# Kernel optimization log

Measured on AMD Instinct MI355X. Metric: run time of the kernel, lower is better.

## Reference

```python
import jax, jax.numpy as jnp
import numpy as np

B, S, H_DIM = 2, 2048, 1024
N_HEADS, HEAD_DIM = 16, 64
EPS = 1e-6


def phi(x):
    return jax.nn.elu(x) + 1.0


def setup_inputs() -> dict:
    key = jax.random.key(0)
    ks = jax.random.split(key, 11)
    std = 0.02
    proj = N_HEADS * HEAD_DIM
    return {
        "query": jax.random.normal(ks[0], (B, S, H_DIM), dtype=jnp.float32),
        "key": jax.random.normal(ks[1], (B, S, H_DIM), dtype=jnp.float32),
        "value": jax.random.normal(ks[2], (B, S, H_DIM), dtype=jnp.float32),
        "Wq": jax.random.normal(ks[3], (proj, H_DIM), dtype=jnp.float32) * std,
        "bq": jnp.zeros((proj,), dtype=jnp.float32),
        "Wk": jax.random.normal(ks[4], (proj, H_DIM), dtype=jnp.float32) * std,
        "bk": jnp.zeros((proj,), dtype=jnp.float32),
        "Wv": jax.random.normal(ks[5], (proj, H_DIM), dtype=jnp.float32) * std,
        "bv": jnp.zeros((proj,), dtype=jnp.float32),
        "Wo": jax.random.normal(ks[6], (H_DIM, proj), dtype=jnp.float32) * std,
        "bo": jnp.zeros((H_DIM,), dtype=jnp.float32),
    }


def reference(query, key, value, Wq, bq, Wk, bk, Wv, bv, Wo, bo):
    b, s, _ = query.shape
    # QKV projections (torch nn.Linear: y = x @ W.T + b)
    q = query @ Wq.T + bq
    k = key @ Wk.T + bk
    v = value @ Wv.T + bv
    # (b, s, h*d) -> (b, h, s, d)
    def split_heads(t):
        return t.reshape(b, s, N_HEADS, HEAD_DIM).transpose(0, 2, 1, 3)
    q, k, v = split_heads(q), split_heads(k), split_heads(v)

    q_phi = phi(q)  # (b,h,s,d)
    k_phi = phi(k)

    # cumulative outer products: (b,h,s,d_k,d_v)
    kv = k_phi[..., :, None] * v[..., None, :]
    kv_cumsum = jnp.cumsum(kv, axis=2)
    k_phi_cumsum = jnp.cumsum(k_phi, axis=2)

    out_num = jnp.einsum('bhsd,bhsdj->bhsj', q_phi, kv_cumsum)
    out_den = jnp.einsum('bhsd,bhsd->bhs', q_phi, k_phi_cumsum)
    out = out_num / (out_den[..., None] + EPS)

    out = out.transpose(0, 2, 1, 3).reshape(b, s, N_HEADS * HEAD_DIM)
    return out @ Wo.T + bo
```

## Files before the change

kernel.cpp:

```cpp
#include <hip/hip_runtime.h>
#include <hip/hip_bf16.h>
#include <stdint.h>

typedef __bf16 bf16x8 __attribute__((ext_vector_type(8)));
typedef float  f32x4  __attribute__((ext_vector_type(4)));
typedef __hip_bfloat16 hbf16;

#define AS1 __attribute__((address_space(1)))
#define AS3 __attribute__((address_space(3)))

__device__ __forceinline__ void gload_lds16(const void* g, void* l) {
  __builtin_amdgcn_global_load_lds((const AS1 void*)g, (AS3 void*)l, 16, 0, 0);
}

__device__ __forceinline__ f32x4 mfma_bf16(bf16x8 a, bf16x8 b, f32x4 c) {
  return __builtin_amdgcn_mfma_f32_16x16x32_bf16(a, b, c, 0, 0, 0);
}


__global__ __launch_bounds__(256) void convert_all(
    const float* __restrict__ q, const float* __restrict__ k, const float* __restrict__ v,
    const float* __restrict__ wq, const float* __restrict__ wk,
    const float* __restrict__ wv, const float* __restrict__ wo,
    hbf16* __restrict__ dst)
{
  const int i8 = (blockIdx.x * 256 + threadIdx.x) * 8;
  const float* src;
  int off;
  if      (i8 < (4  << 20)) { src = q;  off = i8; }
  else if (i8 < (8  << 20)) { src = k;  off = i8 - (4  << 20); }
  else if (i8 < (12 << 20)) { src = v;  off = i8 - (8  << 20); }
  else if (i8 < (13 << 20)) { src = wq; off = i8 - (12 << 20); }
  else if (i8 < (14 << 20)) { src = wk; off = i8 - (13 << 20); }
  else if (i8 < (15 << 20)) { src = wv; off = i8 - (14 << 20); }
  else                      { src = wo; off = i8 - (15 << 20); }
  const float4 a = *(const float4*)(src + off);
  const float4 b = *(const float4*)(src + off + 4);
  hbf16 h[8];
  h[0] = __float2bfloat16(a.x); h[1] = __float2bfloat16(a.y);
  h[2] = __float2bfloat16(a.z); h[3] = __float2bfloat16(a.w);
  h[4] = __float2bfloat16(b.x); h[5] = __float2bfloat16(b.y);
  h[6] = __float2bfloat16(b.z); h[7] = __float2bfloat16(b.w);
  *(uint4*)(dst + i8) = *(uint4*)h;
}

__device__ __forceinline__ void gemm_core_128(
    const hbf16* __restrict__ A, const hbf16* __restrict__ Bw,
    int by, int bx, hbf16* sA, hbf16* sB, f32x4 (&acc)[4][4])
{
  const int tid  = threadIdx.x;
  const int lane = tid & 63;
  const int wid  = tid >> 6;
  const int wm = wid >> 1, wn = wid & 1;
  const int l15 = lane & 15, l4 = lane >> 4;
  const int K = 1024;

  auto STAGE = [&](int kt) {
    const int k0 = kt * 64;
    #pragma unroll
    for (int j = 0; j < 4; ++j) {
      const int o   = (j * 256 + tid) * 16;
      const int row = o >> 7;
      const int csw = (o & 127) ^ ((row & 7) << 4);
      gload_lds16((const char*)A  + ((size_t)(by * 128 + row) * K + k0) * 2 + csw,
                  (char*)sA + o);
      gload_lds16((const char*)Bw + ((size_t)(bx * 128 + row) * K + k0) * 2 + csw,
                  (char*)sB + o);
    }
  };

  STAGE(0);
  for (int kt = 0; kt < 16; ++kt) {
    __syncthreads();
    bf16x8 af[2][4], bfr[2][4];
    #pragma unroll
    for (int kk = 0; kk < 2; ++kk) {
      #pragma unroll
      for (int m = 0; m < 4; ++m) {
        const int row = wm * 64 + m * 16 + l15;
        const int col = (kk * 64 + l4 * 16) ^ ((row & 7) << 4);
        af[kk][m] = *(const bf16x8*)((const char*)sA + row * 128 + col);
      }
      #pragma unroll
      for (int n = 0; n < 4; ++n) {
        const int row = wn * 64 + n * 16 + l15;
        const int col = (kk * 64 + l4 * 16) ^ ((row & 7) << 4);
        bfr[kk][n] = *(const bf16x8*)((const char*)sB + row * 128 + col);
      }
    }
    __syncthreads();
    if (kt < 15) STAGE(kt + 1);
    __builtin_amdgcn_sched_barrier(0);
    #pragma unroll
    for (int kk = 0; kk < 2; ++kk) {
      #pragma unroll
      for (int m = 0; m < 4; ++m) {
        #pragma unroll
        for (int n = 0; n < 4; ++n) {
          acc[m][n] = mfma_bf16(af[kk][m], bfr[kk][n], acc[m][n]);
        }
      }
    }
  }
}

__device__ __forceinline__ void xcd_remap(int& bx, int& by) {
  const int X = blockIdx.x, Y = blockIdx.y;
  by = X * 4 + (Y & 3);
  bx = Y >> 2;
}

__global__ __launch_bounds__(256, 3) void qkv_gemm(
    const hbf16* __restrict__ qin, const hbf16* __restrict__ kin, const hbf16* __restrict__ vin,
    const hbf16* __restrict__ wq, const hbf16* __restrict__ wk, const hbf16* __restrict__ wv,
    const float* __restrict__ bq, const float* __restrict__ bk, const float* __restrict__ bv,
    hbf16* __restrict__ q_phi, hbf16* __restrict__ k_phi,
    hbf16* __restrict__ kphiT, hbf16* __restrict__ vT)
{
  const int z = blockIdx.z;
  const hbf16* A    = (z == 0) ? qin : (z == 1) ? kin : vin;
  const hbf16* W    = (z == 0) ? wq  : (z == 1) ? wk  : wv;
  const float* bias = (z == 0) ? bq  : (z == 1) ? bk  : bv;

  int bx, by;
  xcd_remap(bx, by);

  __shared__ hbf16 sA[128 * 64];
  __shared__ hbf16 sB[128 * 64];
  f32x4 acc[4][4] = {};
  gemm_core_128(A, W, by, bx, sA, sB, acc);

  const int tid = threadIdx.x, lane = tid & 63, wid = tid >> 6;
  const int wm = wid >> 1, wn = wid & 1, l15 = lane & 15, l4 = lane >> 4;

  #pragma unroll
  for (int n = 0; n < 4; ++n) {
    const int gn = bx * 128 + wn * 64 + n * 16 + l15;
    const float bs = bias[gn];
    const int h = gn >> 6, dd = gn & 63;
    #pragma unroll
    for (int m = 0; m < 4; ++m) {
      #pragma unroll
      for (int j = 0; j < 4; ++j) {
        const int gm = by * 128 + wm * 64 + m * 16 + l4 * 4 + j;
        const int b = gm >> 11, s = gm & 2047;
        float val = acc[m][n][j] + bs;
        if (z < 2) val = (val > 0.f) ? (val + 1.f) : __expf(val);
        const hbf16 hv = __float2bfloat16(val);
        const int bh = b * 16 + h;
        if (z == 0) {
          q_phi[((size_t)bh * 2048 + s) * 64 + dd] = hv;
        } else if (z == 1) {
          k_phi[((size_t)bh * 2048 + s) * 64 + dd] = hv;
          kphiT[((size_t)bh * 32 + (s >> 6)) * 4096 + dd * 64 + (s & 63)] = hv;
        } else {
          vT[((size_t)bh * 32 + (s >> 6)) * 4096 + dd * 64 + (s & 63)] = hv;
        }
      }
    }
  }
}

__global__ __launch_bounds__(256) void chunk_sums(
    const hbf16* __restrict__ kphiT, const hbf16* __restrict__ vT,
    float* __restrict__ sums)
{
  const int c = blockIdx.x, bh = blockIdx.y;
  const int tid = threadIdx.x, lane = tid & 63, w = tid >> 6;
  const int l15 = lane & 15, l4 = lane >> 4;
  const size_t tbase = ((size_t)bh * 32 + c) * 4096;

  f32x4 acc[5] = {};
  #pragma unroll
  for (int kk = 0; kk < 2; ++kk) {
    const bf16x8 bfr = *(const bf16x8*)&kphiT[tbase + (w * 16 + l15) * 64 + l4 * 8 + kk * 32];
    #pragma unroll
    for (int mj = 0; mj < 5; ++mj) {
      bf16x8 af;
      if (mj < 4) {
        af = *(const bf16x8*)&vT[tbase + (mj * 16 + l15) * 64 + l4 * 8 + kk * 32];
      } else {
        const __bf16 e = (l15 == 0) ? (__bf16)1.0f : (__bf16)0.0f;
        #pragma unroll
        for (int i = 0; i < 8; ++i) af[i] = e;
      }
      acc[mj] = mfma_bf16(af, bfr, acc[mj]);
    }
  }
  float* outp = sums + ((size_t)bh * 32 + c) * 5120;
  #pragma unroll
  for (int mj = 0; mj < 5; ++mj) {
    #pragma unroll
    for (int j = 0; j < 4; ++j) {
      outp[(mj * 16 + l4 * 4 + j) * 64 + w * 16 + l15] = acc[mj][j];
    }
  }
}

__global__ __launch_bounds__(256) void chunk_scan(
    const float* __restrict__ sums, hbf16* __restrict__ pre)
{
  const int elem = blockIdx.x * 256 + threadIdx.x;
  const int bh = blockIdx.y;
  const size_t base = (size_t)bh * 32 * 5120 + elem;
  float v[32];
  #pragma unroll
  for (int c = 0; c < 32; ++c) v[c] = sums[base + (size_t)c * 5120];
  float run = 0.f;
  #pragma unroll
  for (int c = 0; c < 32; ++c) {
    pre[base + (size_t)c * 5120] = __float2bfloat16(run);
    run += v[c];
  }
}

__global__ __launch_bounds__(256) void attn_chunk(
    const hbf16* __restrict__ q_phi, const hbf16* __restrict__ k_phi,
    const hbf16* __restrict__ vT, const hbf16* __restrict__ pre,
    hbf16* __restrict__ attn)
{
  const int c = blockIdx.x, bh = blockIdx.y;
  const int tid = threadIdx.x, lane = tid & 63, w = tid >> 6;
  const int l15 = lane & 15, l4 = lane >> 4;
  __shared__ hbf16 sS[4 * 16 * 64];

  const size_t qbase = ((size_t)bh * 2048 + c * 64) * 64;
  const size_t tbase = ((size_t)bh * 32 + c) * 4096;
  const size_t pbase = ((size_t)bh * 32 + c) * 5120;

  bf16x8 aq[2];
  #pragma unroll
  for (int kk = 0; kk < 2; ++kk)
    aq[kk] = *(const bf16x8*)&q_phi[qbase + (w * 16 + l15) * 64 + l4 * 8 + kk * 32];

  f32x4 accS[4] = {};
  #pragma unroll
  for (int kk = 0; kk < 2; ++kk) {
    #pragma unroll
    for (int ni = 0; ni < 4; ++ni) {
      const bf16x8 bk = *(const bf16x8*)&k_phi[qbase + (ni * 16 + l15) * 64 + l4 * 8 + kk * 32];
      accS[ni] = mfma_bf16(aq[kk], bk, accS[ni]);
    }
  }
  #pragma unroll
  for (int ni = 0; ni < 4; ++ni) {
    #pragma unroll
    for (int j = 0; j < 4; ++j) {
      const int r  = l4 * 4 + j;
      const int cc = ni * 16 + l15;
      const float v = (cc <= w * 16 + r) ? accS[ni][j] : 0.f;
      sS[w * 1024 + r * 64 + (cc ^ ((r & 7) << 3))] = __float2bfloat16(v);
    }
  }

  f32x4 accN[5] = {};
  #pragma unroll
  for (int kk = 0; kk < 2; ++kk) {
    const bf16x8 aS = *(const bf16x8*)&sS[w * 1024 + l15 * 64 +
                                          ((l4 * 8 + kk * 32) ^ ((l15 & 7) << 3))];
    #pragma unroll
    for (int ni = 0; ni < 5; ++ni) {
      bf16x8 bv;
      if (ni < 4) {
        bv = *(const bf16x8*)&vT[tbase + (ni * 16 + l15) * 64 + l4 * 8 + kk * 32];
      } else {
        const __bf16 e = (l15 == 0) ? (__bf16)1.0f : (__bf16)0.0f;
        #pragma unroll
        for (int i = 0; i < 8; ++i) bv[i] = e;
      }
      accN[ni] = mfma_bf16(aS, bv, accN[ni]);
    }
  }
  #pragma unroll
  for (int kk = 0; kk < 2; ++kk) {
    #pragma unroll
    for (int ni = 0; ni < 5; ++ni) {
      const bf16x8 bp = *(const bf16x8*)&pre[pbase + (ni * 16 + l15) * 64 + l4 * 8 + kk * 32];
      accN[ni] = mfma_bf16(aq[kk], bp, accN[ni]);
    }
  }
  const int b = bh >> 4, h = bh & 15;
  #pragma unroll
  for (int j = 0; j < 4; ++j) {
    const float den = __shfl(accN[4][j], lane & 48);
    const float inv = 1.f / (den + 1e-6f);
    const int sg = c * 64 + w * 16 + l4 * 4 + j;
    #pragma unroll
    for (int ni = 0; ni < 4; ++ni) {
      attn[((size_t)b * 2048 + sg) * 1024 + h * 64 + ni * 16 + l15] =
          __float2bfloat16(accN[ni][j] * inv);
    }
  }
}

__global__ __launch_bounds__(256, 3) void out_gemm(
    const hbf16* __restrict__ attn, const hbf16* __restrict__ wo,
    const float* __restrict__ bo, float* __restrict__ out)
{
  int bx, by;
  xcd_remap(bx, by);

  __shared__ hbf16 sA[128 * 64];
  __shared__ hbf16 sB[128 * 64];
  f32x4 acc[4][4] = {};
  gemm_core_128(attn, wo, by, bx, sA, sB, acc);

  const int tid = threadIdx.x, lane = tid & 63, wid = tid >> 6;
  const int wm = wid >> 1, wn = wid & 1, l15 = lane & 15, l4 = lane >> 4;
  #pragma unroll
  for (int n = 0; n < 4; ++n) {
    const int gn = bx * 128 + wn * 64 + n * 16 + l15;
    const float bs = bo[gn];
    #pragma unroll
    for (int m = 0; m < 4; ++m) {
      #pragma unroll
      for (int j = 0; j < 4; ++j) {
        const int gm = by * 128 + wm * 64 + m * 16 + l4 * 4 + j;
        out[(size_t)gm * 1024 + gn] = acc[m][n][j] + bs;
      }
    }
  }
}

extern "C" void kernel_launch(void* const* d_in, const int* in_sizes, int n_in,
                              void* d_out, int out_size, void* d_ws, size_t ws_size,
                              hipStream_t stream) {
  const float* q  = (const float*)d_in[0];
  const float* k  = (const float*)d_in[1];
  const float* v  = (const float*)d_in[2];
  const float* Wq = (const float*)d_in[3];
  const float* bq = (const float*)d_in[4];
  const float* Wk = (const float*)d_in[5];
  const float* bk = (const float*)d_in[6];
  const float* Wv = (const float*)d_in[7];
  const float* bv = (const float*)d_in[8];
  const float* Wo = (const float*)d_in[9];
  const float* bo = (const float*)d_in[10];

  char* ws = (char*)d_ws;
  const size_t MB = (size_t)1 << 20;
  hbf16* qin  = (hbf16*)(ws + 0 * MB);
  hbf16* kin  = (hbf16*)(ws + 8 * MB);
  hbf16* vin  = (hbf16*)(ws + 16 * MB);
  hbf16* wqb  = (hbf16*)(ws + 24 * MB);
  hbf16* wkb  = (hbf16*)(ws + 26 * MB);
  hbf16* wvb  = (hbf16*)(ws + 28 * MB);
  hbf16* wob  = (hbf16*)(ws + 30 * MB);
  hbf16* qphi = (hbf16*)(ws + 32 * MB);
  hbf16* kphi = (hbf16*)(ws + 40 * MB);
  hbf16* kphT = (hbf16*)(ws + 48 * MB);
  hbf16* vTb  = (hbf16*)(ws + 56 * MB);
  hbf16* attn = (hbf16*)(ws + 64 * MB);
  float* sums = (float*)(ws + 72 * MB);
  hbf16* pre  = (hbf16*)(ws + 92 * MB);

  convert_all<<<8192, 256, 0, stream>>>(q, k, v, Wq, Wk, Wv, Wo, qin);
  qkv_gemm<<<dim3(8, 32, 3), 256, 0, stream>>>(qin, kin, vin, wqb, wkb, wvb,
                                               bq, bk, bv, qphi, kphi, kphT, vTb);
  chunk_sums<<<dim3(32, 32), 256, 0, stream>>>(kphT, vTb, sums);
  chunk_scan<<<dim3(20, 32), 256, 0, stream>>>(sums, pre);
  attn_chunk<<<dim3(32, 32), 256, 0, stream>>>(qphi, kphi, vTb, pre, attn);
  out_gemm<<<dim3(8, 32), 256, 0, stream>>>(attn, wob, bo, (float*)d_out);
}
```

Baseline: 201.4 us.

## Use 64x128 double-buffered GEMM tiles with async prefetch in QKV and output GEMMs

```diff
diff --git a/kernel.cpp b/kernel.cpp
--- a/kernel.cpp
+++ b/kernel.cpp
@@ -44,70 +44,89 @@
   *(uint4*)(dst + i8) = *(uint4*)h;
 }
 
-__device__ __forceinline__ void gemm_core_128(
+template<int NKT>
+__device__ __forceinline__ void gemm_core_64x128(
     const hbf16* __restrict__ A, const hbf16* __restrict__ Bw,
-    int by, int bx, hbf16* sA, hbf16* sB, f32x4 (&acc)[4][4])
+    int by, int bx, hbf16* sA, hbf16* sB, f32x4 (&acc)[4][2])
 {
   const int tid  = threadIdx.x;
   const int lane = tid & 63;
   const int wid  = tid >> 6;
-  const int wm = wid >> 1, wn = wid & 1;
-  const int l15 = lane & 15, l4 = lane >> 4;
-  const int K = 1024;
-
-  auto STAGE = [&](int kt) {
+  const int l15 = lane & 15, l4 = lane >> 4;
+  const int K = NKT * 64;
+
+  auto STAGE = [&](int kt, int buf) {
     const int k0 = kt * 64;
+    #pragma unroll
+    for (int j = 0; j < 2; ++j) {
+      const int o   = (j * 256 + tid) * 16;
+      const int row = o >> 7;
+      const int csw = (o & 127) ^ ((row & 7) << 4);
+      gload_lds16((const char*)A + ((size_t)(by * 64 + row) * K + k0) * 2 + csw,
+                  (char*)(sA + buf * 64 * 64) + o);
+    }
     #pragma unroll
     for (int j = 0; j < 4; ++j) {
       const int o   = (j * 256 + tid) * 16;
       const int row = o >> 7;
       const int csw = (o & 127) ^ ((row & 7) << 4);
-      gload_lds16((const char*)A  + ((size_t)(by * 128 + row) * K + k0) * 2 + csw,
-                  (char*)sA + o);
       gload_lds16((const char*)Bw + ((size_t)(bx * 128 + row) * K + k0) * 2 + csw,
-                  (char*)sB + o);
+                  (char*)(sB + buf * 128 * 64) + o);
     }
   };
 
-  STAGE(0);
-  for (int kt = 0; kt < 16; ++kt) {
-    __syncthreads();
-    bf16x8 af[2][4], bfr[2][4];
+  STAGE(0, 0);
+  STAGE(1, 1);
+  #pragma unroll
+  for (int kt = 0; kt < NKT; ++kt) {
+    const int buf = kt & 1;
+    if (kt < NKT - 1) asm volatile("s_waitcnt vmcnt(6)" ::: "memory");
+    else              asm volatile("s_waitcnt vmcnt(0)" ::: "memory");
+    __builtin_amdgcn_s_barrier();
+    __builtin_amdgcn_sched_barrier(0);
+
+    bf16x8 af[2][4], bfr[2][2];
+    const hbf16* bA = sA + buf * 64 * 64;
+    const hbf16* bB = sB + buf * 128 * 64;
     #pragma unroll
     for (int kk = 0; kk < 2; ++kk) {
       #pragma unroll
       for (int m = 0; m < 4; ++m) {
-        const int row = wm * 64 + m * 16 + l15;
+        const int row = m * 16 + l15;
         const int col = (kk * 64 + l4 * 16) ^ ((row & 7) << 4);
-        af[kk][m] = *(const bf16x8*)((const char*)sA + row * 128 + col);
-      }
-      #pragma unroll
-      for (int n = 0; n < 4; ++n) {
-        const int row = wn * 64 + n * 16 + l15;
+        af[kk][m] = *(const bf16x8*)((const char*)bA + row * 128 + col);
+      }
+      #pragma unroll
+      for (int n = 0; n < 2; ++n) {
+        const int row = wid * 32 + n * 16 + l15;
         const int col = (kk * 64 + l4 * 16) ^ ((row & 7) << 4);
-        bfr[kk][n] = *(const bf16x8*)((const char*)sB + row * 128 + col);
-      }
-    }
-    __syncthreads();
-    if (kt < 15) STAGE(kt + 1);
+        bfr[kk][n] = *(const bf16x8*)((const char*)bB + row * 128 + col);
+      }
+    }
+    asm volatile("s_waitcnt lgkmcnt(0)" ::: "memory");
     __builtin_amdgcn_sched_barrier(0);
-    #pragma unroll
-    for (int kk = 0; kk < 2; ++kk) {
-      #pragma unroll
-      for (int m = 0; m < 4; ++m) {
+    if (kt + 2 < NKT) {
+      __builtin_amdgcn_s_barrier();
+      __builtin_amdgcn_sched_barrier(0);
+      STAGE(kt + 2, buf);
+      __builtin_amdgcn_sched_barrier(0);
+    }
+    __builtin_amdgcn_s_setprio(1);
+    #pragma unroll
+    for (int kk = 0; kk < 2; ++kk)
+      #pragma unroll
+      for (int m = 0; m < 4; ++m)
         #pragma unroll
-        for (int n = 0; n < 4; ++n) {
+        for (int n = 0; n < 2; ++n)
           acc[m][n] = mfma_bf16(af[kk][m], bfr[kk][n], acc[m][n]);
-        }
-      }
-    }
+    __builtin_amdgcn_s_setprio(0);
   }
 }
 
 __device__ __forceinline__ void xcd_remap(int& bx, int& by) {
   const int X = blockIdx.x, Y = blockIdx.y;
-  by = X * 4 + (Y & 3);
-  bx = Y >> 2;
+  by = X * 8 + (Y & 7);
+  bx = Y >> 3;
 }
 
 __global__ __launch_bounds__(256, 3) void qkv_gemm(
@@ -125,24 +144,24 @@
   int bx, by;
   xcd_remap(bx, by);
 
-  __shared__ hbf16 sA[128 * 64];
-  __shared__ hbf16 sB[128 * 64];
-  f32x4 acc[4][4] = {};
-  gemm_core_128(A, W, by, bx, sA, sB, acc);
+  __shared__ hbf16 sA[2 * 64 * 64];
+  __shared__ hbf16 sB[2 * 128 * 64];
+  f32x4 acc[4][2] = {};
+  gemm_core_64x128<16>(A, W, by, bx, sA, sB, acc);
 
   const int tid = threadIdx.x, lane = tid & 63, wid = tid >> 6;
-  const int wm = wid >> 1, wn = wid & 1, l15 = lane & 15, l4 = lane >> 4;
-
-  #pragma unroll
-  for (int n = 0; n < 4; ++n) {
-    const int gn = bx * 128 + wn * 64 + n * 16 + l15;
+  const int l15 = lane & 15, l4 = lane >> 4;
+
+  #pragma unroll
+  for (int n = 0; n < 2; ++n) {
+    const int gn = bx * 128 + wid * 32 + n * 16 + l15;
     const float bs = bias[gn];
     const int h = gn >> 6, dd = gn & 63;
     #pragma unroll
     for (int m = 0; m < 4; ++m) {
       #pragma unroll
       for (int j = 0; j < 4; ++j) {
-        const int gm = by * 128 + wm * 64 + m * 16 + l4 * 4 + j;
+        const int gm = by * 64 + m * 16 + l4 * 4 + j;
         const int b = gm >> 11, s = gm & 2047;
         float val = acc[m][n][j] + bs;
         if (z < 2) val = (val > 0.f) ? (val + 1.f) : __expf(val);
@@ -300,22 +319,22 @@
   int bx, by;
   xcd_remap(bx, by);
 
-  __shared__ hbf16 sA[128 * 64];
-  __shared__ hbf16 sB[128 * 64];
-  f32x4 acc[4][4] = {};
-  gemm_core_128(attn, wo, by, bx, sA, sB, acc);
+  __shared__ hbf16 sA[2 * 64 * 64];
+  __shared__ hbf16 sB[2 * 128 * 64];
+  f32x4 acc[4][2] = {};
+  gemm_core_64x128<16>(attn, wo, by, bx, sA, sB, acc);
 
   const int tid = threadIdx.x, lane = tid & 63, wid = tid >> 6;
-  const int wm = wid >> 1, wn = wid & 1, l15 = lane & 15, l4 = lane >> 4;
-  #pragma unroll
-  for (int n = 0; n < 4; ++n) {
-    const int gn = bx * 128 + wn * 64 + n * 16 + l15;
+  const int l15 = lane & 15, l4 = lane >> 4;
+  #pragma unroll
+  for (int n = 0; n < 2; ++n) {
+    const int gn = bx * 128 + wid * 32 + n * 16 + l15;
     const float bs = bo[gn];
     #pragma unroll
     for (int m = 0; m < 4; ++m) {
       #pragma unroll
       for (int j = 0; j < 4; ++j) {
-        const int gm = by * 128 + wm * 64 + m * 16 + l4 * 4 + j;
+        const int gm = by * 64 + m * 16 + l4 * 4 + j;
         out[(size_t)gm * 1024 + gn] = acc[m][n][j] + bs;
       }
     }
@@ -355,10 +374,10 @@
   hbf16* pre  = (hbf16*)(ws + 92 * MB);
 
   convert_all<<<8192, 256, 0, stream>>>(q, k, v, Wq, Wk, Wv, Wo, qin);
-  qkv_gemm<<<dim3(8, 32, 3), 256, 0, stream>>>(qin, kin, vin, wqb, wkb, wvb,
+  qkv_gemm<<<dim3(8, 64, 3), 256, 0, stream>>>(qin, kin, vin, wqb, wkb, wvb,
                                                bq, bk, bv, qphi, kphi, kphT, vTb);
   chunk_sums<<<dim3(32, 32), 256, 0, stream>>>(kphT, vTb, sums);
   chunk_scan<<<dim3(20, 32), 256, 0, stream>>>(sums, pre);
   attn_chunk<<<dim3(32, 32), 256, 0, stream>>>(qphi, kphi, vTb, pre, attn);
-  out_gemm<<<dim3(8, 32), 256, 0, stream>>>(attn, wob, bo, (float*)d_out);
-}
+  out_gemm<<<dim3(8, 64), 256, 0, stream>>>(attn, wob, bo, (float*)d_out);
+}
```

New measurement: 206.0 us. 1.02x slower.

## Replace QKV projection with 256x256-tile double-buffered 8-wave pipelined GEMM

Applied to the files above, without the earlier changes.

```diff
diff --git a/kernel.cpp b/kernel.cpp
--- a/kernel.cpp
+++ b/kernel.cpp
@@ -44,6 +44,162 @@
   *(uint4*)(dst + i8) = *(uint4*)h;
 }
 
+#define NKT_Q 16
+
+__global__ __launch_bounds__(512, 2) void qkv_gemm256(
+    const hbf16* __restrict__ qin, const hbf16* __restrict__ kin, const hbf16* __restrict__ vin,
+    const hbf16* __restrict__ wq, const hbf16* __restrict__ wk, const hbf16* __restrict__ wv,
+    const float* __restrict__ bq, const float* __restrict__ bk, const float* __restrict__ bv,
+    hbf16* __restrict__ q_phi, hbf16* __restrict__ k_phi,
+    hbf16* __restrict__ kphiT, hbf16* __restrict__ vT)
+{
+  const int p  = blockIdx.x + (blockIdx.y << 2) + (blockIdx.z << 6);
+  const int L  = (p & 7) * 24 + (p >> 3);
+  const int z  = L >> 6;
+  const int rem = L & 63;
+  const int by = rem >> 2;
+  const int bx = rem & 3;
+
+  const hbf16* A    = (z == 0) ? qin : (z == 1) ? kin : vin;
+  const hbf16* W    = (z == 0) ? wq  : (z == 1) ? wk  : wv;
+  const float* bias = (z == 0) ? bq  : (z == 1) ? bk  : bv;
+
+  __shared__ hbf16 sA[2 * 256 * 64];
+  __shared__ hbf16 sB[2 * 256 * 64];
+
+  const int tid  = threadIdx.x;
+  const int lane = tid & 63;
+  const int wid  = tid >> 6;
+  const int wm   = wid >> 2;
+  const int wn   = wid & 3;
+  const int l15  = lane & 15, l4 = lane >> 4;
+  const int K = 1024;
+
+  auto STAGEQ = [&](const hbf16* G, hbf16* S, int gRowBase, int t, int q) {
+    const int o   = tid * 16;
+    const int row = o >> 7;
+    const int csw = (o & 127) ^ ((row & 7) << 4);
+    gload_lds16((const char*)G + ((size_t)(gRowBase + q * 64 + row) * K + t * 64) * 2 + csw,
+                (char*)(S + (t & 1) * (256 * 64) + q * (64 * 64)) + o);
+  };
+
+  f32x4 acc[4][2][4] = {};
+
+  #pragma unroll
+  for (int q = 0; q < 4; ++q) STAGEQ(A, sA, by * 256, 0, q);
+  #pragma unroll
+  for (int q = 0; q < 4; ++q) STAGEQ(W, sB, bx * 256, 0, q);
+  #pragma unroll
+  for (int q = 0; q < 4; ++q) STAGEQ(W, sB, bx * 256, 1, q);
+  STAGEQ(A, sA, by * 256, 1, 0);
+  STAGEQ(A, sA, by * 256, 1, 1);
+  asm volatile("s_waitcnt vmcnt(6)" ::: "memory");
+  __builtin_amdgcn_s_barrier();
+
+  for (int kt = 0; kt < NKT_Q; kt += 2) {
+    #pragma unroll
+    for (int half = 0; half < 2; ++half) {
+      const int t = kt + half;
+      const hbf16* bufA = sA + (t & 1) * (256 * 64);
+      const hbf16* bufB = sB + (t & 1) * (256 * 64);
+      bf16x8 bf[4][2];
+      #pragma unroll
+      for (int pph = 0; pph < 4; ++pph) {
+        if (pph == 0) {
+          #pragma unroll
+          for (int n = 0; n < 4; ++n)
+            #pragma unroll
+            for (int kk = 0; kk < 2; ++kk) {
+              const int row = wn * 64 + n * 16 + l15;
+              const int col = (kk * 64 + l4 * 16) ^ ((row & 7) << 4);
+              bf[n][kk] = *(const bf16x8*)((const char*)bufB + row * 128 + col);
+            }
+        }
+        bf16x8 af[2][2];
+        #pragma unroll
+        for (int i = 0; i < 2; ++i)
+          #pragma unroll
+          for (int kk = 0; kk < 2; ++kk) {
+            const int row = pph * 64 + wm * 32 + i * 16 + l15;
+            const int col = (kk * 64 + l4 * 16) ^ ((row & 7) << 4);
+            af[i][kk] = *(const bf16x8*)((const char*)bufA + row * 128 + col);
+          }
+        if (half == 0) {
+          if (pph == 0) {
+            STAGEQ(A, sA, by * 256, kt + 1, 2);
+            STAGEQ(A, sA, by * 256, kt + 1, 3);
+          } else if (kt + 2 < NKT_Q) {
+            if (pph == 1) { STAGEQ(W, sB, bx * 256, kt + 2, 0); STAGEQ(W, sB, bx * 256, kt + 2, 1); }
+            if (pph == 2) { STAGEQ(W, sB, bx * 256, kt + 2, 2); STAGEQ(W, sB, bx * 256, kt + 2, 3); }
+            if (pph == 3) { STAGEQ(A, sA, by * 256, kt + 2, 0); STAGEQ(A, sA, by * 256, kt + 2, 1); }
+          }
+        } else {
+          if (pph == 0) {
+            if (kt + 2 < NKT_Q) {
+              STAGEQ(A, sA, by * 256, kt + 2, 2);
+              STAGEQ(A, sA, by * 256, kt + 2, 3);
+            }
+          } else if (kt + 3 < NKT_Q) {
+            if (pph == 1) { STAGEQ(W, sB, bx * 256, kt + 3, 0); STAGEQ(W, sB, bx * 256, kt + 3, 1); }
+            if (pph == 2) { STAGEQ(W, sB, bx * 256, kt + 3, 2); STAGEQ(W, sB, bx * 256, kt + 3, 3); }
+            if (pph == 3) { STAGEQ(A, sA, by * 256, kt + 3, 0); STAGEQ(A, sA, by * 256, kt + 3, 1); }
+          }
+        }
+        __builtin_amdgcn_s_barrier();
+        asm volatile("s_waitcnt lgkmcnt(0)" ::: "memory");
+        __builtin_amdgcn_s_setprio(1);
+        #pragma unroll
+        for (int i = 0; i < 2; ++i)
+          #pragma unroll
+          for (int n = 0; n < 4; ++n)
+            #pragma unroll
+            for (int kk = 0; kk < 2; ++kk)
+              acc[pph][i][n] = mfma_bf16(af[i][kk], bf[n][kk], acc[pph][i][n]);
+        __builtin_amdgcn_s_setprio(0);
+        if (pph == 3) {
+          if (half == 0) {
+            if (kt + 2 < NKT_Q) asm volatile("s_waitcnt vmcnt(6)" ::: "memory");
+            else                asm volatile("s_waitcnt vmcnt(0)" ::: "memory");
+          } else {
+            if (kt + 2 < NKT_Q) asm volatile("s_waitcnt vmcnt(6)" ::: "memory");
+          }
+        }
+        __builtin_amdgcn_s_barrier();
+      }
+    }
+  }
+
+  #pragma unroll
+  for (int n = 0; n < 4; ++n) {
+    const int gn = bx * 256 + wn * 64 + n * 16 + l15;
+    const float bs = bias[gn];
+    const int h = gn >> 6, dd = gn & 63;
+    #pragma unroll
+    for (int pph = 0; pph < 4; ++pph) {
+      #pragma unroll
+      for (int i = 0; i < 2; ++i) {
+        #pragma unroll
+        for (int j = 0; j < 4; ++j) {
+          const int gm = by * 256 + pph * 64 + wm * 32 + i * 16 + l4 * 4 + j;
+          const int b = gm >> 11, s = gm & 2047;
+          float val = acc[pph][i][n][j] + bs;
+          if (z < 2) val = (val > 0.f) ? (val + 1.f) : __expf(val);
+          const hbf16 hv = __float2bfloat16(val);
+          const int bh = b * 16 + h;
+          if (z == 0) {
+            q_phi[((size_t)bh * 2048 + s) * 64 + dd] = hv;
+          } else if (z == 1) {
+            k_phi[((size_t)bh * 2048 + s) * 64 + dd] = hv;
+            kphiT[((size_t)bh * 32 + (s >> 6)) * 4096 + dd * 64 + (s & 63)] = hv;
+          } else {
+            vT[((size_t)bh * 32 + (s >> 6)) * 4096 + dd * 64 + (s & 63)] = hv;
+          }
+        }
+      }
+    }
+  }
+}
+
 __device__ __forceinline__ void gemm_core_128(
     const hbf16* __restrict__ A, const hbf16* __restrict__ Bw,
     int by, int bx, hbf16* sA, hbf16* sB, f32x4 (&acc)[4][4])
@@ -92,15 +248,12 @@
     if (kt < 15) STAGE(kt + 1);
     __builtin_amdgcn_sched_barrier(0);
     #pragma unroll
-    for (int kk = 0; kk < 2; ++kk) {
-      #pragma unroll
-      for (int m = 0; m < 4; ++m) {
-        #pragma unroll
-        for (int n = 0; n < 4; ++n) {
+    for (int kk = 0; kk < 2; ++kk)
+      #pragma unroll
+      for (int m = 0; m < 4; ++m)
+        #pragma unroll
+        for (int n = 0; n < 4; ++n)
           acc[m][n] = mfma_bf16(af[kk][m], bfr[kk][n], acc[m][n]);
-        }
-      }
-    }
   }
 }
 
@@ -108,57 +261,6 @@
   const int X = blockIdx.x, Y = blockIdx.y;
   by = X * 4 + (Y & 3);
   bx = Y >> 2;
-}
-
-__global__ __launch_bounds__(256, 3) void qkv_gemm(
-    const hbf16* __restrict__ qin, const hbf16* __restrict__ kin, const hbf16* __restrict__ vin,
-    const hbf16* __restrict__ wq, const hbf16* __restrict__ wk, const hbf16* __restrict__ wv,
-    const float* __restrict__ bq, const float* __restrict__ bk, const float* __restrict__ bv,
-    hbf16* __restrict__ q_phi, hbf16* __restrict__ k_phi,
-    hbf16* __restrict__ kphiT, hbf16* __restrict__ vT)
-{
-  const int z = blockIdx.z;
-  const hbf16* A    = (z == 0) ? qin : (z == 1) ? kin : vin;
-  const hbf16* W    = (z == 0) ? wq  : (z == 1) ? wk  : wv;
-  const float* bias = (z == 0) ? bq  : (z == 1) ? bk  : bv;
-
-  int bx, by;
-  xcd_remap(bx, by);
-
-  __shared__ hbf16 sA[128 * 64];
-  __shared__ hbf16 sB[128 * 64];
-  f32x4 acc[4][4] = {};
-  gemm_core_128(A, W, by, bx, sA, sB, acc);
-
-  const int tid = threadIdx.x, lane = tid & 63, wid = tid >> 6;
-  const int wm = wid >> 1, wn = wid & 1, l15 = lane & 15, l4 = lane >> 4;
-
-  #pragma unroll
-  for (int n = 0; n < 4; ++n) {
-    const int gn = bx * 128 + wn * 64 + n * 16 + l15;
-    const float bs = bias[gn];
-    const int h = gn >> 6, dd = gn & 63;
-    #pragma unroll
-    for (int m = 0; m < 4; ++m) {
-      #pragma unroll
-      for (int j = 0; j < 4; ++j) {
-        const int gm = by * 128 + wm * 64 + m * 16 + l4 * 4 + j;
-        const int b = gm >> 11, s = gm & 2047;
-        float val = acc[m][n][j] + bs;
-        if (z < 2) val = (val > 0.f) ? (val + 1.f) : __expf(val);
-        const hbf16 hv = __float2bfloat16(val);
-        const int bh = b * 16 + h;
-        if (z == 0) {
-          q_phi[((size_t)bh * 2048 + s) * 64 + dd] = hv;
-        } else if (z == 1) {
-          k_phi[((size_t)bh * 2048 + s) * 64 + dd] = hv;
-          kphiT[((size_t)bh * 32 + (s >> 6)) * 4096 + dd * 64 + (s & 63)] = hv;
-        } else {
-          vT[((size_t)bh * 32 + (s >> 6)) * 4096 + dd * 64 + (s & 63)] = hv;
-        }
-      }
-    }
-  }
 }
 
 __global__ __launch_bounds__(256) void chunk_sums(
@@ -355,8 +457,8 @@
   hbf16* pre  = (hbf16*)(ws + 92 * MB);
 
   convert_all<<<8192, 256, 0, stream>>>(q, k, v, Wq, Wk, Wv, Wo, qin);
-  qkv_gemm<<<dim3(8, 32, 3), 256, 0, stream>>>(qin, kin, vin, wqb, wkb, wvb,
-                                               bq, bk, bv, qphi, kphi, kphT, vTb);
+  qkv_gemm256<<<dim3(4, 16, 3), 512, 0, stream>>>(qin, kin, vin, wqb, wkb, wvb,
+                                                  bq, bk, bv, qphi, kphi, kphT, vTb);
   chunk_sums<<<dim3(32, 32), 256, 0, stream>>>(kphT, vTb, sums);
   chunk_scan<<<dim3(20, 32), 256, 0, stream>>>(sums, pre);
   attn_chunk<<<dim3(32, 32), 256, 0, stream>>>(qphi, kphi, vTb, pre, attn);
```

Measured after the change: 226.4 us. 12.4% more time.

## Stage QKV and attention epilogues through LDS for coalesced 16-byte stores

Applied to the files above, without the earlier changes.

```diff
diff --git a/kernel.cpp b/kernel.cpp
--- a/kernel.cpp
+++ b/kernel.cpp
@@ -92,15 +92,12 @@
     if (kt < 15) STAGE(kt + 1);
     __builtin_amdgcn_sched_barrier(0);
     #pragma unroll
-    for (int kk = 0; kk < 2; ++kk) {
-      #pragma unroll
-      for (int m = 0; m < 4; ++m) {
+    for (int kk = 0; kk < 2; ++kk)
+      #pragma unroll
+      for (int m = 0; m < 4; ++m)
         #pragma unroll
-        for (int n = 0; n < 4; ++n) {
+        for (int n = 0; n < 4; ++n)
           acc[m][n] = mfma_bf16(af[kk][m], bfr[kk][n], acc[m][n]);
-        }
-      }
-    }
   }
 }
 
@@ -125,38 +122,77 @@
   int bx, by;
   xcd_remap(bx, by);
 
-  __shared__ hbf16 sA[128 * 64];
-  __shared__ hbf16 sB[128 * 64];
+  __shared__ hbf16 smem[2 * 128 * 64];
   f32x4 acc[4][4] = {};
-  gemm_core_128(A, W, by, bx, sA, sB, acc);
+  gemm_core_128(A, W, by, bx, smem, smem + 128 * 64, acc);
 
   const int tid = threadIdx.x, lane = tid & 63, wid = tid >> 6;
   const int wm = wid >> 1, wn = wid & 1, l15 = lane & 15, l4 = lane >> 4;
-
-  #pragma unroll
-  for (int n = 0; n < 4; ++n) {
-    const int gn = bx * 128 + wn * 64 + n * 16 + l15;
-    const float bs = bias[gn];
-    const int h = gn >> 6, dd = gn & 63;
-    #pragma unroll
-    for (int m = 0; m < 4; ++m) {
-      #pragma unroll
-      for (int j = 0; j < 4; ++j) {
-        const int gm = by * 128 + wm * 64 + m * 16 + l4 * 4 + j;
-        const int b = gm >> 11, s = gm & 2047;
-        float val = acc[m][n][j] + bs;
-        if (z < 2) val = (val > 0.f) ? (val + 1.f) : __expf(val);
-        const hbf16 hv = __float2bfloat16(val);
-        const int bh = b * 16 + h;
-        if (z == 0) {
-          q_phi[((size_t)bh * 2048 + s) * 64 + dd] = hv;
-        } else if (z == 1) {
-          k_phi[((size_t)bh * 2048 + s) * 64 + dd] = hv;
-          kphiT[((size_t)bh * 32 + (s >> 6)) * 4096 + dd * 64 + (s & 63)] = hv;
-        } else {
-          vT[((size_t)bh * 32 + (s >> 6)) * 4096 + dd * 64 + (s & 63)] = hv;
+  const int b = by >> 4;
+
+  float bs[4];
+  #pragma unroll
+  for (int n = 0; n < 4; ++n) bs[n] = bias[bx * 128 + wn * 64 + n * 16 + l15];
+
+  auto finish = [&](float v) -> float {
+    return (z < 2) ? ((v > 0.f) ? (v + 1.f) : __expf(v)) : v;
+  };
+
+  if (z < 2) {
+    #pragma unroll
+    for (int n = 0; n < 4; ++n) {
+      const int col = wn * 64 + n * 16 + l15;
+      #pragma unroll
+      for (int m = 0; m < 4; ++m) {
+        #pragma unroll
+        for (int j = 0; j < 4; ++j) {
+          const int row = wm * 64 + m * 16 + l4 * 4 + j;
+          smem[row * 128 + (col ^ ((row & 7) << 3))] =
+              __float2bfloat16(finish(acc[m][n][j] + bs[n]));
         }
       }
+    }
+    __syncthreads();
+    hbf16* dst = (z == 0) ? q_phi : k_phi;
+    #pragma unroll
+    for (int it = 0; it < 8; ++it) {
+      const int sgi = it * 256 + tid;
+      const int sl = sgi >> 4, seg = sgi & 15;
+      const uint4 vv = *(const uint4*)&smem[sl * 128 + ((seg * 8) ^ ((sl & 7) << 3))];
+      const int gnb = bx * 128 + seg * 8;
+      const int h = gnb >> 6, dd = gnb & 63;
+      const int s = (by * 128 + sl) & 2047;
+      *(uint4*)&dst[(((size_t)(b * 16 + h)) * 2048 + s) * 64 + dd] = vv;
+    }
+  }
+  if (z >= 1) {
+    if (z == 1) __syncthreads();
+    #pragma unroll
+    for (int n = 0; n < 4; ++n) {
+      const int gnl = wn * 64 + n * 16 + l15;
+      const int x = (gnl & 7) << 3;
+      #pragma unroll
+      for (int m = 0; m < 4; ++m) {
+        const int s0 = wm * 64 + m * 16 + l4 * 4;
+        hbf16 pk[4];
+        #pragma unroll
+        for (int j = 0; j < 4; ++j)
+          pk[j] = __float2bfloat16(finish(acc[m][n][j] + bs[n]));
+        *(ushort4*)&smem[gnl * 128 + (s0 ^ x)] = *(ushort4*)pk;
+      }
+    }
+    __syncthreads();
+    hbf16* dst = (z == 1) ? kphiT : vT;
+    #pragma unroll
+    for (int it = 0; it < 8; ++it) {
+      const int sgi = it * 256 + tid;
+      const int gn = sgi >> 4, sseg = sgi & 15;
+      const uint4 vv = *(const uint4*)&smem[gn * 128 + ((sseg * 8) ^ ((gn & 7) << 3))];
+      const int gnb = bx * 128 + gn;
+      const int h = gnb >> 6, dd = gnb & 63;
+      const int sg = by * 128 + sseg * 8;
+      const int c = (sg & 2047) >> 6, sin = sg & 63;
+      *(uint4*)&dst[(((size_t)(b * 16 + h)) * 32 + c) * 4096 + dd * 64 + sin] = vv;
     }
   }
 }
@@ -284,12 +320,20 @@
   for (int j = 0; j < 4; ++j) {
     const float den = __shfl(accN[4][j], lane & 48);
     const float inv = 1.f / (den + 1e-6f);
-    const int sg = c * 64 + w * 16 + l4 * 4 + j;
+    const int sl = w * 16 + l4 * 4 + j;
     #pragma unroll
     for (int ni = 0; ni < 4; ++ni) {
-      attn[((size_t)b * 2048 + sg) * 1024 + h * 64 + ni * 16 + l15] =
+      sS[sl * 64 + ((ni * 16 + l15) ^ ((sl & 7) << 3))] =
           __float2bfloat16(accN[ni][j] * inv);
     }
+  }
+  __syncthreads();
+  #pragma unroll
+  for (int it = 0; it < 2; ++it) {
+    const int sgi = it * 256 + tid;
+    const int sl = sgi >> 3, seg = sgi & 7;
+    const uint4 vv = *(const uint4*)&sS[sl * 64 + ((seg * 8) ^ ((sl & 7) << 3))];
+    *(uint4*)&attn[((size_t)b * 2048 + c * 64 + sl) * 1024 + h * 64 + seg * 8] = vv;
   }
 }
 
@@ -300,10 +344,9 @@
   int bx, by;
   xcd_remap(bx, by);
 
-  __shared__ hbf16 sA[128 * 64];
-  __shared__ hbf16 sB[128 * 64];
+  __shared__ hbf16 smem[2 * 128 * 64];
   f32x4 acc[4][4] = {};
-  gemm_core_128(attn, wo, by, bx, sA, sB, acc);
+  gemm_core_128(attn, wo, by, bx, smem, smem + 128 * 64, acc);
 
   const int tid = threadIdx.x, lane = tid & 63, wid = tid >> 6;
   const int wm = wid >> 1, wn = wid & 1, l15 = lane & 15, l4 = lane >> 4;
```

Measured after the change: 196.4 us. 1.03x faster.
